# Performance work log

Hardware: AMD Instinct MI355X
Metric: run time of the kernel (lower is better)

## Reference

```python
import jax, jax.numpy as jnp
import numpy as np

NUM_HEADS = 16
LN_EPS = 1e-5


def setup_inputs() -> dict:
    key = jax.random.key(0)
    ks = jax.random.split(key, 6)
    b, s, d = 2, 2048, 1024
    scale = 1.0 / np.sqrt(d)
    return {
        "x": jax.random.normal(ks[0], (b, s, d), dtype=jnp.float32),
        "W_w": jax.random.normal(ks[1], (3 * d, d), dtype=jnp.float32) * scale,
        "W_b": jax.random.normal(ks[2], (3 * d,), dtype=jnp.float32) * 0.01,
        "proj_w": jax.random.normal(ks[3], (d, d), dtype=jnp.float32) * scale,
        "proj_b": jax.random.normal(ks[4], (d,), dtype=jnp.float32) * 0.01,
        "gamma": jnp.ones((d,), dtype=jnp.float32),
        "beta": jnp.zeros((d,), dtype=jnp.float32),
    }


def reference(x, W_w, W_b, proj_w, proj_b, gamma, beta):
    b, s, d = x.shape
    h = NUM_HEADS
    hd = d // h
    # fused QKV projection: [b,s,3d]
    qkv = x @ W_w.T + W_b
    q, k, v = jnp.split(qkv, 3, axis=-1)
    # [b,s,d] -> [b,h,s,hd]
    q, k, v = (z.reshape(b, s, h, hd).transpose(0, 2, 1, 3) for z in (q, k, v))
    # NOTE: original scales by sqrt(d), not sqrt(head_dim)
    attn = jnp.einsum('bhqd,bhkd->bhqk', q, k) / jnp.sqrt(jnp.asarray(d, x.dtype))
    attn_weights = jax.nn.softmax(attn, axis=-1)  # [b,h,s,s]
    o = jnp.einsum('bhqk,bhkd->bhqd', attn_weights, v)
    o = o.transpose(0, 2, 1, 3).reshape(b, s, d)
    out = o @ proj_w.T + proj_b  # dropout is identity at eval
    y = x + out
    mu = jnp.mean(y, axis=-1, keepdims=True)
    var = jnp.var(y, axis=-1, keepdims=True)
    y_norm = (y - mu) / jnp.sqrt(var + LN_EPS) * gamma + beta
    return (y_norm, attn_weights)
```

## Files before the change

kernel.cpp:

```cpp
#include <hip/hip_runtime.h>
#include <cstdint>

#define BB 2
#define SS 2048
#define DD 1024
#define HH 16
#define HDIM 64
#define MM (BB*SS)
#define N3 (3*DD)

typedef __attribute__((ext_vector_type(4))) float f32x4;
typedef __attribute__((ext_vector_type(8))) __bf16 bf16x8;

static __device__ __forceinline__ unsigned short f2bf_fast(float f) {
  __bf16 h = (__bf16)f;
  return __builtin_bit_cast(unsigned short, h);
}

static __device__ __forceinline__ uint4 pack8f(const float4 a, const float4 b) {
  union { unsigned short us[8]; uint4 v; } pk;
  pk.us[0] = f2bf_fast(a.x); pk.us[1] = f2bf_fast(a.y); pk.us[2] = f2bf_fast(a.z); pk.us[3] = f2bf_fast(a.w);
  pk.us[4] = f2bf_fast(b.x); pk.us[5] = f2bf_fast(b.y); pk.us[6] = f2bf_fast(b.z); pk.us[7] = f2bf_fast(b.w);
  return pk.v;
}

static __device__ __forceinline__ void gload16(const unsigned short* g, unsigned short* l) {
  __builtin_amdgcn_global_load_lds(
      (const __attribute__((address_space(1))) void*)g,
      (__attribute__((address_space(3))) void*)l, 16, 0, 0);
}

__global__ __launch_bounds__(256) void cvt_kernel(
    const float* __restrict__ x, const float* __restrict__ Ww,
    const float* __restrict__ pw,
    unsigned short* __restrict__ xb, unsigned short* __restrict__ Wwb,
    unsigned short* __restrict__ pwb) {
  const size_t i = ((size_t)blockIdx.x * 256 + threadIdx.x) * 8;
  const float* src;
  unsigned short* dst;
  if (i < 4194304u)       { src = x  + i;            dst = xb  + i; }
  else if (i < 7340032u)  { src = Ww + (i - 4194304u); dst = Wwb + (i - 4194304u); }
  else                    { src = pw + (i - 7340032u); dst = pwb + (i - 7340032u); }
  const float4* s4 = (const float4*)src;
  *(uint4*)dst = pack8f(s4[0], s4[1]);
}

__global__ __launch_bounds__(256) void gemm_qkv(
    const unsigned short* __restrict__ xb, const unsigned short* __restrict__ Wwb,
    const float* __restrict__ Wb,
    unsigned short* __restrict__ qb, unsigned short* __restrict__ kb,
    unsigned short* __restrict__ vbT) {
  __shared__ __align__(16) unsigned short Sh[128 * 132];
  unsigned short* As = Sh;
  unsigned short* Bs = Sh + 128 * 32;
  const int t = threadIdx.x;
  const int l = t & 63, w = t >> 6;
  const int wr = w >> 1, wc = w & 1;
  const int m0 = blockIdx.y * 128, n0 = blockIdx.x * 128;
  f32x4 acc[4][4] = {};

  for (int kt = 0; kt < DD; kt += 32) {
    __syncthreads();
    #pragma unroll
    for (int i = 0; i < 2; ++i) {
      const int row = (i * 4 + w) * 16 + (l >> 2);
      const int cc = (l & 3) * 8;
      gload16(xb  + (size_t)(m0 + row) * DD + kt + cc, &As[(i * 4 + w) * 512]);
      gload16(Wwb + (size_t)(n0 + row) * DD + kt + cc, &Bs[(i * 4 + w) * 512]);
    }
    __syncthreads();
    bf16x8 a[4], b[4];
    #pragma unroll
    for (int i = 0; i < 4; ++i) {
      a[i] = __builtin_bit_cast(bf16x8, *(const uint4*)&As[(wr * 64 + i * 16 + (l & 15)) * 32 + (l >> 4) * 8]);
      b[i] = __builtin_bit_cast(bf16x8, *(const uint4*)&Bs[(wc * 64 + i * 16 + (l & 15)) * 32 + (l >> 4) * 8]);
    }
    #pragma unroll
    for (int i = 0; i < 4; ++i)
      #pragma unroll
      for (int j = 0; j < 4; ++j)
        acc[i][j] = __builtin_amdgcn_mfma_f32_16x16x32_bf16(a[i], b[j], acc[i][j], 0, 0, 0);
  }
  __syncthreads();

  if (n0 < 2048) {
    const bool isq = (n0 < 1024);
    #pragma unroll
    for (int i = 0; i < 4; ++i)
      #pragma unroll
      for (int j = 0; j < 4; ++j)
        #pragma unroll
        for (int r = 0; r < 4; ++r) {
          const int row = m0 + wr * 64 + i * 16 + (l >> 4) * 4 + r;
          const int col = n0 + wc * 64 + j * 16 + (l & 15);
          const float v = acc[i][j][r] + Wb[col];
          const int bidx = row >> 11, srow = row & 2047;
          const int cc = col & 1023, head = cc >> 6, hd = cc & 63;
          const size_t idx = ((size_t)((bidx * HH + head) * SS + srow)) * HDIM + hd;
          if (isq) qb[idx] = f2bf_fast(v * 0.04508422f);
          else     kb[idx] = f2bf_fast(v);
        }
  } else {
    unsigned short* Tt = Sh;
    #pragma unroll
    for (int i = 0; i < 4; ++i)
      #pragma unroll
      for (int j = 0; j < 4; ++j)
        #pragma unroll
        for (int r = 0; r < 4; ++r) {
          const int rr = wr * 64 + i * 16 + (l >> 4) * 4 + r;
          const int cl = wc * 64 + j * 16 + (l & 15);
          Tt[rr * 132 + cl] = f2bf_fast(acc[i][j][r] + Wb[n0 + cl]);
        }
    __syncthreads();
    const int bidx = m0 >> 11, srow0 = m0 & 2047;
    const int q = t & 3;
    #pragma unroll
    for (int ci = 0; ci < 2; ++ci) {
      const int c = ci * 64 + (t >> 2);
      const int vcol = n0 - 2048 + c;
      const int head = vcol >> 6, hd = vcol & 63;
      unsigned short* dst = vbT + ((size_t)(bidx * HH + head) * HDIM + hd) * SS + srow0;
      #pragma unroll
      for (int e8 = 0; e8 < 4; ++e8) {
        const int r0 = e8 * 32 + q * 8;
        union { unsigned short us[8]; uint4 v; } pk;
        #pragma unroll
        for (int e = 0; e < 8; ++e) pk.us[e] = Tt[(r0 + e) * 132 + c];
        *(uint4*)(dst + r0) = pk.v;
      }
    }
  }
}

__global__ __launch_bounds__(256) void attn_kernel(
    const unsigned short* __restrict__ qb,
    const unsigned short* __restrict__ kb,
    const unsigned short* __restrict__ vbT,
    unsigned short* __restrict__ ob,
    float* __restrict__ attn_out) {
  __shared__ float Ored[4][64][68];
  __shared__ float Lred[4][64];
  const int t = threadIdx.x;
  const int l = t & 63, w = t >> 6;
  const int q_l = l & 15, hi = l >> 4;
  const int bid = blockIdx.x;
  const int swz = (bid & 7) * 128 + (bid >> 3);
  const int bh = swz >> 5;
  const int q0 = (swz & 31) * 64;
  const size_t base = (size_t)bh * SS * HDIM;

  bf16x8 qa[4][2];
  #pragma unroll
  for (int j = 0; j < 4; ++j)
    #pragma unroll
    for (int kc = 0; kc < 2; ++kc)
      qa[j][kc] = __builtin_bit_cast(bf16x8,
          *(const uint4*)(qb + base + (size_t)(q0 + j * 16 + q_l) * HDIM + kc * 32 + hi * 8));

  const unsigned short* kga = kb + base + (size_t)(w * 16 + q_l) * HDIM + hi * 8;
  const unsigned short* vga = vbT + ((size_t)bh * HDIM + q_l) * SS + w * 16 + hi * 4;

  float lsum[4] = {0.f, 0.f, 0.f, 0.f};
  {
    uint4 k0 = *(const uint4*)(kga);
    uint4 k1 = *(const uint4*)(kga + 32);
    for (int kt = 0; kt < SS; kt += 64) {
      const bool more = (kt + 64) < SS;
      uint4 n0, n1;
      if (more) {
        n0 = *(const uint4*)(kga + (size_t)(kt + 64) * HDIM);
        n1 = *(const uint4*)(kga + (size_t)(kt + 64) * HDIM + 32);
      }
      f32x4 sQ[4] = {};
      const bf16x8 kf0 = __builtin_bit_cast(bf16x8, k0);
      const bf16x8 kf1 = __builtin_bit_cast(bf16x8, k1);
      __builtin_amdgcn_s_setprio(1);
      #pragma unroll
      for (int j = 0; j < 4; ++j) {
        sQ[j] = __builtin_amdgcn_mfma_f32_16x16x32_bf16(kf0, qa[j][0], sQ[j], 0, 0, 0);
        sQ[j] = __builtin_amdgcn_mfma_f32_16x16x32_bf16(kf1, qa[j][1], sQ[j], 0, 0, 0);
      }
      __builtin_amdgcn_s_setprio(0);
      #pragma unroll
      for (int j = 0; j < 4; ++j)
        #pragma unroll
        for (int r = 0; r < 4; ++r)
          lsum[j] += __builtin_amdgcn_exp2f(sQ[j][r]);
      k0 = n0; k1 = n1;
    }
  }
  #pragma unroll
  for (int j = 0; j < 4; ++j) {
    float s = lsum[j];
    s += __shfl_xor(s, 16);
    s += __shfl_xor(s, 32);
    lsum[j] = s;
  }
  if (hi == 0) {
    #pragma unroll
    for (int j = 0; j < 4; ++j) Lred[w][j * 16 + q_l] = lsum[j];
  }
  __syncthreads();
  float rl[4];
  #pragma unroll
  for (int j = 0; j < 4; ++j)
    rl[j] = 1.0f / (Lred[0][j * 16 + q_l] + Lred[1][j * 16 + q_l] +
                    Lred[2][j * 16 + q_l] + Lred[3][j * 16 + q_l]);

  float* pbs[4];
  #pragma unroll
  for (int j = 0; j < 4; ++j)
    pbs[j] = attn_out + ((size_t)bh * SS + (q0 + j * 16 + q_l)) * SS + w * 16 + hi * 4;

  f32x4 of[4][4] = {};
  {
    uint4 k0 = *(const uint4*)(kga);
    uint4 k1 = *(const uint4*)(kga + 32);
    uint2 vv[4];
    #pragma unroll
    for (int d4 = 0; d4 < 4; ++d4)
      vv[d4] = *(const uint2*)(vga + (size_t)(d4 * 16) * SS);
    for (int kt = 0; kt < SS; kt += 64) {
      const bool more = (kt + 64) < SS;
      uint4 n0, n1; uint2 nv[4];
      if (more) {
        n0 = *(const uint4*)(kga + (size_t)(kt + 64) * HDIM);
        n1 = *(const uint4*)(kga + (size_t)(kt + 64) * HDIM + 32);
        #pragma unroll
        for (int d4 = 0; d4 < 4; ++d4)
          nv[d4] = *(const uint2*)(vga + (size_t)(d4 * 16) * SS + kt + 64);
      }
      f32x4 sQ[4] = {};
      const bf16x8 kf0 = __builtin_bit_cast(bf16x8, k0);
      const bf16x8 kf1 = __builtin_bit_cast(bf16x8, k1);
      __builtin_amdgcn_s_setprio(1);
      #pragma unroll
      for (int j = 0; j < 4; ++j) {
        sQ[j] = __builtin_amdgcn_mfma_f32_16x16x32_bf16(kf0, qa[j][0], sQ[j], 0, 0, 0);
        sQ[j] = __builtin_amdgcn_mfma_f32_16x16x32_bf16(kf1, qa[j][1], sQ[j], 0, 0, 0);
      }
      __builtin_amdgcn_s_setprio(0);
      bf16x8 pbp[4];
      #pragma unroll
      for (int j = 0; j < 4; ++j) {
        float4 pv;
        pv.x = __builtin_amdgcn_exp2f(sQ[j][0]) * rl[j];
        pv.y = __builtin_amdgcn_exp2f(sQ[j][1]) * rl[j];
        pv.z = __builtin_amdgcn_exp2f(sQ[j][2]) * rl[j];
        pv.w = __builtin_amdgcn_exp2f(sQ[j][3]) * rl[j];
        __builtin_nontemporal_store(*(const f32x4*)&pv, (f32x4*)(pbs[j] + kt));
        union { unsigned short us[8]; uint4 v; } pk;
        pk.us[0] = f2bf_fast(pv.x); pk.us[1] = f2bf_fast(pv.y);
        pk.us[2] = f2bf_fast(pv.z); pk.us[3] = f2bf_fast(pv.w);
        pk.us[4] = 0; pk.us[5] = 0; pk.us[6] = 0; pk.us[7] = 0;
        pbp[j] = __builtin_bit_cast(bf16x8, pk.v);
      }
      __builtin_amdgcn_s_setprio(1);
      #pragma unroll
      for (int d4 = 0; d4 < 4; ++d4) {
        uint4 vp; vp.x = vv[d4].x; vp.y = vv[d4].y; vp.z = 0u; vp.w = 0u;
        const bf16x8 vfp = __builtin_bit_cast(bf16x8, vp);
        #pragma unroll
        for (int j = 0; j < 4; ++j)
          of[d4][j] = __builtin_amdgcn_mfma_f32_16x16x32_bf16(vfp, pbp[j], of[d4][j], 0, 0, 0);
      }
      __builtin_amdgcn_s_setprio(0);
      k0 = n0; k1 = n1;
      #pragma unroll
      for (int d4 = 0; d4 < 4; ++d4) vv[d4] = nv[d4];
    }
  }

  #pragma unroll
  for (int d4 = 0; d4 < 4; ++d4)
    #pragma unroll
    for (int j = 0; j < 4; ++j)
      *(f32x4*)&Ored[w][j * 16 + q_l][d4 * 16 + hi * 4] = of[d4][j];
  __syncthreads();
  const int bidx = bh >> 4, h_ = bh & 15;
  const int qf = w * 16 + q_l;
  union { unsigned short us[16]; uint4 v[2]; } opk;
  #pragma unroll
  for (int c4 = 0; c4 < 4; ++c4) {
    const int d0 = hi * 16 + c4 * 4;
    f32x4 s = *(const f32x4*)&Ored[0][qf][d0];
    s += *(const f32x4*)&Ored[1][qf][d0];
    s += *(const f32x4*)&Ored[2][qf][d0];
    s += *(const f32x4*)&Ored[3][qf][d0];
    opk.us[c4 * 4 + 0] = f2bf_fast(s[0]);
    opk.us[c4 * 4 + 1] = f2bf_fast(s[1]);
    opk.us[c4 * 4 + 2] = f2bf_fast(s[2]);
    opk.us[c4 * 4 + 3] = f2bf_fast(s[3]);
  }
  unsigned short* orow = ob + ((size_t)bidx * SS + (q0 + qf)) * DD + h_ * 64 + hi * 16;
  *(uint4*)orow = opk.v[0];
  *(uint4*)(orow + 8) = opk.v[1];
}

__global__ __launch_bounds__(256) void gemm_proj(
    const unsigned short* __restrict__ ob, const unsigned short* __restrict__ pwb,
    const float* __restrict__ pb, const float* __restrict__ x,
    float* __restrict__ y) {
  __shared__ __align__(16) unsigned short As[128 * 32];
  __shared__ __align__(16) unsigned short Bs[128 * 32];
  const int t = threadIdx.x;
  const int l = t & 63, w = t >> 6;
  const int wr = w >> 1, wc = w & 1;
  const int m0 = blockIdx.y * 128, n0 = blockIdx.x * 128;
  f32x4 acc[4][4] = {};

  for (int kt = 0; kt < DD; kt += 32) {
    __syncthreads();
    #pragma unroll
    for (int i = 0; i < 2; ++i) {
      const int row = (i * 4 + w) * 16 + (l >> 2);
      const int cc = (l & 3) * 8;
      gload16(ob  + (size_t)(m0 + row) * DD + kt + cc, &As[(i * 4 + w) * 512]);
      gload16(pwb + (size_t)(n0 + row) * DD + kt + cc, &Bs[(i * 4 + w) * 512]);
    }
    __syncthreads();
    bf16x8 a[4], b[4];
    #pragma unroll
    for (int i = 0; i < 4; ++i) {
      a[i] = __builtin_bit_cast(bf16x8, *(const uint4*)&As[(wr * 64 + i * 16 + (l & 15)) * 32 + (l >> 4) * 8]);
      b[i] = __builtin_bit_cast(bf16x8, *(const uint4*)&Bs[(wc * 64 + i * 16 + (l & 15)) * 32 + (l >> 4) * 8]);
    }
    #pragma unroll
    for (int i = 0; i < 4; ++i)
      #pragma unroll
      for (int j = 0; j < 4; ++j)
        acc[i][j] = __builtin_amdgcn_mfma_f32_16x16x32_bf16(a[i], b[j], acc[i][j], 0, 0, 0);
  }
  #pragma unroll
  for (int i = 0; i < 4; ++i)
    #pragma unroll
    for (int j = 0; j < 4; ++j)
      #pragma unroll
      for (int r = 0; r < 4; ++r) {
        const int row = m0 + wr * 64 + i * 16 + (l >> 4) * 4 + r;
        const int col = n0 + wc * 64 + j * 16 + (l & 15);
        const size_t idx = (size_t)row * DD + col;
        y[idx] = acc[i][j][r] + pb[col] + x[idx];
      }
}

__global__ __launch_bounds__(256) void ln_kernel(
    float* __restrict__ y, const float* __restrict__ gamma,
    const float* __restrict__ beta) {
  const int row = blockIdx.x;
  const int t = threadIdx.x;
  const float4 v = ((const float4*)(y + (size_t)row * DD))[t];
  float s  = v.x + v.y + v.z + v.w;
  float s2 = v.x * v.x + v.y * v.y + v.z * v.z + v.w * v.w;
  #pragma unroll
  for (int off = 1; off < 64; off <<= 1) { s += __shfl_xor(s, off); s2 += __shfl_xor(s2, off); }
  __shared__ float red[8];
  const int l = t & 63, w = t >> 6;
  if (l == 0) { red[w] = s; red[4 + w] = s2; }
  __syncthreads();
  s  = red[0] + red[1] + red[2] + red[3];
  s2 = red[4] + red[5] + red[6] + red[7];
  const float mu = s * (1.0f / DD);
  const float var = s2 * (1.0f / DD) - mu * mu;
  const float rs = rsqrtf(var + 1e-5f);
  const float4 g  = ((const float4*)gamma)[t];
  const float4 be = ((const float4*)beta)[t];
  float4 o;
  o.x = (v.x - mu) * rs * g.x + be.x;
  o.y = (v.y - mu) * rs * g.y + be.y;
  o.z = (v.z - mu) * rs * g.z + be.z;
  o.w = (v.w - mu) * rs * g.w + be.w;
  ((float4*)(y + (size_t)row * DD))[t] = o;
}

extern "C" void kernel_launch(void* const* d_in, const int* in_sizes, int n_in,
                              void* d_out, int out_size, void* d_ws, size_t ws_size,
                              hipStream_t stream) {
  const float* x     = (const float*)d_in[0];
  const float* Ww    = (const float*)d_in[1];
  const float* Wb    = (const float*)d_in[2];
  const float* Pw    = (const float*)d_in[3];
  const float* Pb    = (const float*)d_in[4];
  const float* gamma = (const float*)d_in[5];
  const float* beta  = (const float*)d_in[6];

  float* out      = (float*)d_out;
  float* y_norm   = out;
  float* attn_out = out + (size_t)MM * DD;

  char* ws = (char*)d_ws;
  unsigned short* qb  = (unsigned short*)(ws);
  unsigned short* kb  = (unsigned short*)(ws +  8388608);
  unsigned short* vbT = (unsigned short*)(ws + 16777216);
  unsigned short* ob  = (unsigned short*)(ws + 25165824);
  unsigned short* xb  = (unsigned short*)(ws + 33554432);
  unsigned short* Wwb = (unsigned short*)(ws + 41943040);
  unsigned short* pwb = (unsigned short*)(ws + 48234496);

  cvt_kernel<<<4096, 256, 0, stream>>>(x, Ww, Pw, xb, Wwb, pwb);
  gemm_qkv<<<dim3(N3 / 128, MM / 128), 256, 0, stream>>>(xb, Wwb, Wb, qb, kb, vbT);
  attn_kernel<<<1024, 256, 0, stream>>>(qb, kb, vbT, ob, attn_out);
  gemm_proj<<<dim3(DD / 128, MM / 128), 256, 0, stream>>>(ob, pwb, Pb, x, y_norm);
  ln_kernel<<<MM, 256, 0, stream>>>(y_norm, gamma, beta);
}
```

Measured before the change: 263.8 us.

## Restructure attention loops to give each wave a contiguous 64-key chunk per 256-key step

```diff
diff --git a/kernel.cpp b/kernel.cpp
--- a/kernel.cpp
+++ b/kernel.cpp
@@ -158,36 +158,32 @@
       qa[j][kc] = __builtin_bit_cast(bf16x8,
           *(const uint4*)(qb + base + (size_t)(q0 + j * 16 + q_l) * HDIM + kc * 32 + hi * 8));
 
-  const unsigned short* kga = kb + base + (size_t)(w * 16 + q_l) * HDIM + hi * 8;
-  const unsigned short* vga = vbT + ((size_t)bh * HDIM + q_l) * SS + w * 16 + hi * 4;
+  const unsigned short* kga = kb + base + (size_t)(w * 64 + q_l) * HDIM + hi * 8;
+  const unsigned short* vga = vbT + ((size_t)bh * HDIM + q_l) * SS + w * 64 + hi * 4;
 
   float lsum[4] = {0.f, 0.f, 0.f, 0.f};
-  {
-    uint4 k0 = *(const uint4*)(kga);
-    uint4 k1 = *(const uint4*)(kga + 32);
-    for (int kt = 0; kt < SS; kt += 64) {
-      const bool more = (kt + 64) < SS;
-      uint4 n0, n1;
-      if (more) {
-        n0 = *(const uint4*)(kga + (size_t)(kt + 64) * HDIM);
-        n1 = *(const uint4*)(kga + (size_t)(kt + 64) * HDIM + 32);
-      }
+  for (int kt = 0; kt < SS; kt += 256) {
+    uint4 kfr[4][2];
+    #pragma unroll
+    for (int n = 0; n < 4; ++n) {
+      kfr[n][0] = *(const uint4*)(kga + (size_t)(kt + n * 16) * HDIM);
+      kfr[n][1] = *(const uint4*)(kga + (size_t)(kt + n * 16) * HDIM + 32);
+    }
+    #pragma unroll
+    for (int j = 0; j < 4; ++j) {
       f32x4 sQ[4] = {};
-      const bf16x8 kf0 = __builtin_bit_cast(bf16x8, k0);
-      const bf16x8 kf1 = __builtin_bit_cast(bf16x8, k1);
       __builtin_amdgcn_s_setprio(1);
       #pragma unroll
-      for (int j = 0; j < 4; ++j) {
-        sQ[j] = __builtin_amdgcn_mfma_f32_16x16x32_bf16(kf0, qa[j][0], sQ[j], 0, 0, 0);
-        sQ[j] = __builtin_amdgcn_mfma_f32_16x16x32_bf16(kf1, qa[j][1], sQ[j], 0, 0, 0);
+      for (int n = 0; n < 4; ++n) {
+        sQ[n] = __builtin_amdgcn_mfma_f32_16x16x32_bf16(__builtin_bit_cast(bf16x8, kfr[n][0]), qa[j][0], sQ[n], 0, 0, 0);
+        sQ[n] = __builtin_amdgcn_mfma_f32_16x16x32_bf16(__builtin_bit_cast(bf16x8, kfr[n][1]), qa[j][1], sQ[n], 0, 0, 0);
       }
       __builtin_amdgcn_s_setprio(0);
       #pragma unroll
-      for (int j = 0; j < 4; ++j)
+      for (int n = 0; n < 4; ++n)
         #pragma unroll
         for (int r = 0; r < 4; ++r)
-          lsum[j] += __builtin_amdgcn_exp2f(sQ[j][r]);
-      k0 = n0; k1 = n1;
+          lsum[j] += __builtin_amdgcn_exp2f(sQ[n][r]);
     }
   }
   #pragma unroll
@@ -211,64 +207,58 @@
   float* pbs[4];
   #pragma unroll
   for (int j = 0; j < 4; ++j)
-    pbs[j] = attn_out + ((size_t)bh * SS + (q0 + j * 16 + q_l)) * SS + w * 16 + hi * 4;
+    pbs[j] = attn_out + ((size_t)bh * SS + (q0 + j * 16 + q_l)) * SS + w * 64 + hi * 4;
 
   f32x4 of[4][4] = {};
-  {
-    uint4 k0 = *(const uint4*)(kga);
-    uint4 k1 = *(const uint4*)(kga + 32);
-    uint2 vv[4];
+  for (int kt = 0; kt < SS; kt += 256) {
+    uint4 kfr[4][2];
+    #pragma unroll
+    for (int n = 0; n < 4; ++n) {
+      kfr[n][0] = *(const uint4*)(kga + (size_t)(kt + n * 16) * HDIM);
+      kfr[n][1] = *(const uint4*)(kga + (size_t)(kt + n * 16) * HDIM + 32);
+    }
+    uint2 vv[4][4];
     #pragma unroll
     for (int d4 = 0; d4 < 4; ++d4)
-      vv[d4] = *(const uint2*)(vga + (size_t)(d4 * 16) * SS);
-    for (int kt = 0; kt < SS; kt += 64) {
-      const bool more = (kt + 64) < SS;
-      uint4 n0, n1; uint2 nv[4];
-      if (more) {
-        n0 = *(const uint4*)(kga + (size_t)(kt + 64) * HDIM);
-        n1 = *(const uint4*)(kga + (size_t)(kt + 64) * HDIM + 32);
-        #pragma unroll
-        for (int d4 = 0; d4 < 4; ++d4)
-          nv[d4] = *(const uint2*)(vga + (size_t)(d4 * 16) * SS + kt + 64);
-      }
+      #pragma unroll
+      for (int n = 0; n < 4; ++n)
+        vv[d4][n] = *(const uint2*)(vga + (size_t)(d4 * 16) * SS + kt + n * 16);
+
+    #pragma unroll
+    for (int j = 0; j < 4; ++j) {
       f32x4 sQ[4] = {};
-      const bf16x8 kf0 = __builtin_bit_cast(bf16x8, k0);
-      const bf16x8 kf1 = __builtin_bit_cast(bf16x8, k1);
       __builtin_amdgcn_s_setprio(1);
       #pragma unroll
-      for (int j = 0; j < 4; ++j) {
-        sQ[j] = __builtin_amdgcn_mfma_f32_16x16x32_bf16(kf0, qa[j][0], sQ[j], 0, 0, 0);
-        sQ[j] = __builtin_amdgcn_mfma_f32_16x16x32_bf16(kf1, qa[j][1], sQ[j], 0, 0, 0);
+      for (int n = 0; n < 4; ++n) {
+        sQ[n] = __builtin_amdgcn_mfma_f32_16x16x32_bf16(__builtin_bit_cast(bf16x8, kfr[n][0]), qa[j][0], sQ[n], 0, 0, 0);
+        sQ[n] = __builtin_amdgcn_mfma_f32_16x16x32_bf16(__builtin_bit_cast(bf16x8, kfr[n][1]), qa[j][1], sQ[n], 0, 0, 0);
       }
       __builtin_amdgcn_s_setprio(0);
       bf16x8 pbp[4];
       #pragma unroll
-      for (int j = 0; j < 4; ++j) {
+      for (int n = 0; n < 4; ++n) {
         float4 pv;
-        pv.x = __builtin_amdgcn_exp2f(sQ[j][0]) * rl[j];
-        pv.y = __builtin_amdgcn_exp2f(sQ[j][1]) * rl[j];
-        pv.z = __builtin_amdgcn_exp2f(sQ[j][2]) * rl[j];
-        pv.w = __builtin_amdgcn_exp2f(sQ[j][3]) * rl[j];
-        __builtin_nontemporal_store(*(const f32x4*)&pv, (f32x4*)(pbs[j] + kt));
+        pv.x = __builtin_amdgcn_exp2f(sQ[n][0]) * rl[j];
+        pv.y = __builtin_amdgcn_exp2f(sQ[n][1]) * rl[j];
+        pv.z = __builtin_amdgcn_exp2f(sQ[n][2]) * rl[j];
+        pv.w = __builtin_amdgcn_exp2f(sQ[n][3]) * rl[j];
+        __builtin_nontemporal_store(*(const f32x4*)&pv, (f32x4*)(pbs[j] + kt + n * 16));
         union { unsigned short us[8]; uint4 v; } pk;
         pk.us[0] = f2bf_fast(pv.x); pk.us[1] = f2bf_fast(pv.y);
         pk.us[2] = f2bf_fast(pv.z); pk.us[3] = f2bf_fast(pv.w);
         pk.us[4] = 0; pk.us[5] = 0; pk.us[6] = 0; pk.us[7] = 0;
-        pbp[j] = __builtin_bit_cast(bf16x8, pk.v);
+        pbp[n] = __builtin_bit_cast(bf16x8, pk.v);
       }
       __builtin_amdgcn_s_setprio(1);
       #pragma unroll
-      for (int d4 = 0; d4 < 4; ++d4) {
-        uint4 vp; vp.x = vv[d4].x; vp.y = vv[d4].y; vp.z = 0u; vp.w = 0u;
-        const bf16x8 vfp = __builtin_bit_cast(bf16x8, vp);
-        #pragma unroll
-        for (int j = 0; j < 4; ++j)
-          of[d4][j] = __builtin_amdgcn_mfma_f32_16x16x32_bf16(vfp, pbp[j], of[d4][j], 0, 0, 0);
-      }
+      for (int d4 = 0; d4 < 4; ++d4)
+        #pragma unroll
+        for (int n = 0; n < 4; ++n) {
+          uint4 vp; vp.x = vv[d4][n].x; vp.y = vv[d4][n].y; vp.z = 0u; vp.w = 0u;
+          of[d4][j] = __builtin_amdgcn_mfma_f32_16x16x32_bf16(
+              __builtin_bit_cast(bf16x8, vp), pbp[n], of[d4][j], 0, 0, 0);
+        }
       __builtin_amdgcn_s_setprio(0);
-      k0 = n0; k1 = n1;
-      #pragma unroll
-      for (int d4 = 0; d4 < 4; ++d4) vv[d4] = nv[d4];
     }
   }
 
```

Result: slower. 270.7 us (+2.6%).

## Fuse output projection GEMM with residual add and LayerNorm in one kernel

Applied to the files above, without the earlier changes.

```diff
diff --git a/kernel.cpp b/kernel.cpp
--- a/kernel.cpp
+++ b/kernel.cpp
@@ -298,80 +298,92 @@
   *(uint4*)(orow + 8) = opk.v[1];
 }
 
-__global__ __launch_bounds__(256) void gemm_proj(
+__global__ __launch_bounds__(512) void gemm_proj_ln(
     const unsigned short* __restrict__ ob, const unsigned short* __restrict__ pwb,
     const float* __restrict__ pb, const float* __restrict__ x,
-    float* __restrict__ y) {
-  __shared__ __align__(16) unsigned short As[128 * 32];
-  __shared__ __align__(16) unsigned short Bs[128 * 32];
+    const float* __restrict__ gamma, const float* __restrict__ beta,
+    float* __restrict__ out) {
+  __shared__ __align__(16) unsigned short As[16 * 32];
+  __shared__ __align__(16) unsigned short Bs[1024 * 32];
+  __shared__ float gs[1024], bs2[1024];
+  __shared__ float Sred[8][16], S2red[8][16];
   const int t = threadIdx.x;
   const int l = t & 63, w = t >> 6;
-  const int wr = w >> 1, wc = w & 1;
-  const int m0 = blockIdx.y * 128, n0 = blockIdx.x * 128;
-  f32x4 acc[4][4] = {};
-
+  const int q_l = l & 15, hi = l >> 4;
+  const int m0 = blockIdx.x * 16;
+
+  for (int i = t; i < 1024; i += 512) { gs[i] = gamma[i]; bs2[i] = beta[i]; }
+
+  f32x4 acc[8] = {};
   for (int kt = 0; kt < DD; kt += 32) {
     __syncthreads();
-    #pragma unroll
-    for (int i = 0; i < 2; ++i) {
-      const int row = (i * 4 + w) * 16 + (l >> 2);
-      const int cc = (l & 3) * 8;
-      gload16(ob  + (size_t)(m0 + row) * DD + kt + cc, &As[(i * 4 + w) * 512]);
-      gload16(pwb + (size_t)(n0 + row) * DD + kt + cc, &Bs[(i * 4 + w) * 512]);
+    if (w == 0)
+      gload16(ob + (size_t)(m0 + (l >> 2)) * DD + kt + (l & 3) * 8, As);
+    #pragma unroll
+    for (int it = 0; it < 8; ++it) {
+      const int row = (it * 8 + w) * 16 + (l >> 2);
+      gload16(pwb + (size_t)row * DD + kt + (l & 3) * 8, &Bs[(it * 8 + w) * 512]);
     }
     __syncthreads();
-    bf16x8 a[4], b[4];
-    #pragma unroll
-    for (int i = 0; i < 4; ++i) {
-      a[i] = __builtin_bit_cast(bf16x8, *(const uint4*)&As[(wr * 64 + i * 16 + (l & 15)) * 32 + (l >> 4) * 8]);
-      b[i] = __builtin_bit_cast(bf16x8, *(const uint4*)&Bs[(wc * 64 + i * 16 + (l & 15)) * 32 + (l >> 4) * 8]);
-    }
-    #pragma unroll
-    for (int i = 0; i < 4; ++i)
-      #pragma unroll
-      for (int j = 0; j < 4; ++j)
-        acc[i][j] = __builtin_amdgcn_mfma_f32_16x16x32_bf16(a[i], b[j], acc[i][j], 0, 0, 0);
-  }
-  #pragma unroll
-  for (int i = 0; i < 4; ++i)
-    #pragma unroll
-    for (int j = 0; j < 4; ++j)
-      #pragma unroll
-      for (int r = 0; r < 4; ++r) {
-        const int row = m0 + wr * 64 + i * 16 + (l >> 4) * 4 + r;
-        const int col = n0 + wc * 64 + j * 16 + (l & 15);
-        const size_t idx = (size_t)row * DD + col;
-        y[idx] = acc[i][j][r] + pb[col] + x[idx];
-      }
-}
-
-__global__ __launch_bounds__(256) void ln_kernel(
-    float* __restrict__ y, const float* __restrict__ gamma,
-    const float* __restrict__ beta) {
-  const int row = blockIdx.x;
-  const int t = threadIdx.x;
-  const float4 v = ((const float4*)(y + (size_t)row * DD))[t];
-  float s  = v.x + v.y + v.z + v.w;
-  float s2 = v.x * v.x + v.y * v.y + v.z * v.z + v.w * v.w;
-  #pragma unroll
-  for (int off = 1; off < 64; off <<= 1) { s += __shfl_xor(s, off); s2 += __shfl_xor(s2, off); }
-  __shared__ float red[8];
-  const int l = t & 63, w = t >> 6;
-  if (l == 0) { red[w] = s; red[4 + w] = s2; }
+    const bf16x8 a = __builtin_bit_cast(bf16x8, *(const uint4*)&As[q_l * 32 + hi * 8]);
+    #pragma unroll
+    for (int j = 0; j < 8; ++j) {
+      const bf16x8 b = __builtin_bit_cast(bf16x8,
+          *(const uint4*)&Bs[(w * 128 + j * 16 + q_l) * 32 + hi * 8]);
+      acc[j] = __builtin_amdgcn_mfma_f32_16x16x32_bf16(a, b, acc[j], 0, 0, 0);
+    }
+  }
+
+  float s[4] = {0.f, 0.f, 0.f, 0.f}, s2[4] = {0.f, 0.f, 0.f, 0.f};
+  #pragma unroll
+  for (int j = 0; j < 8; ++j) {
+    const int col = w * 128 + j * 16 + q_l;
+    const float pbc = pb[col];
+    #pragma unroll
+    for (int r = 0; r < 4; ++r) {
+      const int row = m0 + hi * 4 + r;
+      const float v = acc[j][r] + pbc + x[(size_t)row * DD + col];
+      acc[j][r] = v;
+      s[r] += v; s2[r] += v * v;
+    }
+  }
+  #pragma unroll
+  for (int r = 0; r < 4; ++r) {
+    #pragma unroll
+    for (int off = 1; off < 16; off <<= 1) {
+      s[r]  += __shfl_xor(s[r], off);
+      s2[r] += __shfl_xor(s2[r], off);
+    }
+  }
+  if (q_l == 0) {
+    #pragma unroll
+    for (int r = 0; r < 4; ++r) {
+      Sred[w][hi * 4 + r]  = s[r];
+      S2red[w][hi * 4 + r] = s2[r];
+    }
+  }
   __syncthreads();
-  s  = red[0] + red[1] + red[2] + red[3];
-  s2 = red[4] + red[5] + red[6] + red[7];
-  const float mu = s * (1.0f / DD);
-  const float var = s2 * (1.0f / DD) - mu * mu;
-  const float rs = rsqrtf(var + 1e-5f);
-  const float4 g  = ((const float4*)gamma)[t];
-  const float4 be = ((const float4*)beta)[t];
-  float4 o;
-  o.x = (v.x - mu) * rs * g.x + be.x;
-  o.y = (v.y - mu) * rs * g.y + be.y;
-  o.z = (v.z - mu) * rs * g.z + be.z;
-  o.w = (v.w - mu) * rs * g.w + be.w;
-  ((float4*)(y + (size_t)row * DD))[t] = o;
+  float mu[4], rs[4];
+  #pragma unroll
+  for (int r = 0; r < 4; ++r) {
+    const int row16 = hi * 4 + r;
+    float ts = 0.f, ts2 = 0.f;
+    #pragma unroll
+    for (int ww = 0; ww < 8; ++ww) { ts += Sred[ww][row16]; ts2 += S2red[ww][row16]; }
+    mu[r] = ts * (1.0f / DD);
+    const float var = ts2 * (1.0f / DD) - mu[r] * mu[r];
+    rs[r] = rsqrtf(var + 1e-5f);
+  }
+  #pragma unroll
+  for (int j = 0; j < 8; ++j) {
+    const int col = w * 128 + j * 16 + q_l;
+    const float g = gs[col], be = bs2[col];
+    #pragma unroll
+    for (int r = 0; r < 4; ++r) {
+      const int row = m0 + hi * 4 + r;
+      out[(size_t)row * DD + col] = (acc[j][r] - mu[r]) * rs[r] * g + be;
+    }
+  }
 }
 
 extern "C" void kernel_launch(void* const* d_in, const int* in_sizes, int n_in,
@@ -401,6 +413,5 @@
   cvt_kernel<<<4096, 256, 0, stream>>>(x, Ww, Pw, xb, Wwb, pwb);
   gemm_qkv<<<dim3(N3 / 128, MM / 128), 256, 0, stream>>>(xb, Wwb, Wb, qb, kb, vbT);
   attn_kernel<<<1024, 256, 0, stream>>>(qb, kb, vbT, ob, attn_out);
-  gemm_proj<<<dim3(DD / 128, MM / 128), 256, 0, stream>>>(ob, pwb, Pb, x, y_norm);
-  ln_kernel<<<MM, 256, 0, stream>>>(y_norm, gamma, beta);
-}
+  gemm_proj_ln<<<MM / 16, 512, 0, stream>>>(ob, pwb, Pb, x, gamma, beta, y_norm);
+}
```

New measurement: 287.8 us. 1.09x slower.
